# Kernel tuning notes

Measured on AMD Instinct MI355X. Metric: run time of the kernel, lower is better.

## Reference

```python
import jax, jax.numpy as jnp
import numpy as np

N = 25000      # nodes
E = 400000     # directed edges (avg degree 16)
FN = 32        # node feature dim
FE = 16        # edge feature dim
H = 16         # hidden_state_size
M = 16         # message_size
ITERS = 3      # mp_iterations


def setup_inputs() -> dict:
    key = jax.random.key(0)
    ks = jax.random.split(key, 16)
    s = 0.1
    return {
        "node_features": jax.random.normal(ks[0], (N, FN), jnp.float32),
        "edge_features": jax.random.normal(ks[1], (E, FE), jnp.float32),
        # Initial dense
        "W_init": jax.random.normal(ks[2], (FN, H), jnp.float32) * s,
        "b_init": jnp.zeros((H,), jnp.float32),
        # edge_net dense: FE -> M*H
        "W_edge": jax.random.normal(ks[3], (FE, M * H), jnp.float32) * s,
        "b_edge": jnp.zeros((M * H,), jnp.float32),
        # GRU (keras default, reset_after=True), input dim 1, units H, gate order z|r|h
        "Wi_gru": jax.random.normal(ks[4], (1, 3 * H), jnp.float32) * s,
        "Wh_gru": jax.random.normal(ks[5], (H, 3 * H), jnp.float32) * s,
        "bi_gru": jnp.zeros((3 * H,), jnp.float32),
        "bh_gru": jnp.zeros((3 * H,), jnp.float32),
        # Readout denses -> 1 output
        "W_ri": jax.random.normal(ks[6], (2 * H, 1), jnp.float32) * s,
        "b_ri": jnp.zeros((1,), jnp.float32),
        "W_rj": jax.random.normal(ks[7], (H, 1), jnp.float32) * s,
        "b_rj": jnp.zeros((1,), jnp.float32),
        # graph structure (directed edges): message to `receivers[e]` from `senders[e]`
        "receivers": jax.random.randint(ks[8], (E,), 0, N, jnp.int32),
        "senders": jax.random.randint(ks[9], (E,), 0, N, jnp.int32),
    }


def _gru_seq(seq, Wi, Wh, bi, bh):
    # seq: [N, T] sequence of scalars per node; keras GRU, reset_after=True, units=H
    n = seq.shape[0]
    xs = seq.T[:, :, None]  # [T, N, 1]
    h0 = jnp.zeros((n, H), seq.dtype)

    def step(h, x_t):
        gx = x_t @ Wi + bi            # [N, 3H]
        gh = h @ Wh + bh              # [N, 3H]
        xz, xr, xh = jnp.split(gx, 3, axis=1)
        hz, hr, hh = jnp.split(gh, 3, axis=1)
        z = jax.nn.sigmoid(xz + hz)
        r = jax.nn.sigmoid(xr + hr)
        hcand = jnp.tanh(xh + r * hh)
        h_new = z * h + (1.0 - z) * hcand
        return h_new, None

    h_final, _ = jax.lax.scan(step, h0, xs)
    return h_final


def reference(node_features, edge_features, W_init, b_init, W_edge, b_edge,
              Wi_gru, Wh_gru, bi_gru, bh_gru, W_ri, b_ri, W_rj, b_rj,
              receivers, senders):
    # Initial hidden state
    hidden0 = node_features @ W_init + b_init   # [N, H]
    hidden = hidden0

    # edge_net(edge) reshaped to per-edge matrices [E, M, H] (constant across iterations)
    edge_mats = (edge_features @ W_edge + b_edge).reshape(E, M, H)

    for _ in range(ITERS):
        h_nb = hidden[senders]                                  # [E, H]
        msg = jnp.einsum("emh,eh->em", edge_mats, h_nb)        # [E, M] matvec per edge
        messages = jax.ops.segment_sum(msg, receivers, num_segments=N)  # sum aggregation
        seq = jnp.concatenate([hidden, messages], axis=1)       # [N, H+M]
        hidden = _gru_seq(seq, Wi_gru, Wh_gru, bi_gru, bh_gru)  # [N, H]

    # Readout
    i = jnp.concatenate([hidden, hidden0], axis=1) @ W_ri + b_ri  # [N, 1]
    j = hidden @ W_rj + b_rj                                      # [N, 1]
    return jnp.sum(i * j, axis=0)                                 # [1]
```

## Files before the change

kernel.cpp:

```cpp
#include <hip/hip_runtime.h>

#define N_NODES 25000
#define N_EDGES 400000

__device__ __forceinline__ float fast_sigmoid(float x) {
    return __builtin_amdgcn_rcpf(1.0f + __expf(-x));
}
__device__ __forceinline__ float fast_tanh(float x) {
    return 1.0f - 2.0f * __builtin_amdgcn_rcpf(__expf(2.0f * x) + 1.0f);
}

#define SWZF(x, k) __int_as_float(__builtin_amdgcn_ds_swizzle(__float_as_int(x), ((k) << 10) | 0x1F))
#define BCAST16(x, t) __int_as_float(__builtin_amdgcn_ds_swizzle(__float_as_int(x), ((t) << 5) | 0x10))

#define STEPK2(k0, k1) { \
        float va = SWZF(hn, k0); float vb = SWZF(hn, k1); \
        az0 = fmaf(va, Wz[k0], az0); az1 = fmaf(vb, Wz[k1], az1); \
        ar0 = fmaf(va, Wr[k0], ar0); ar1 = fmaf(vb, Wr[k1], ar1); \
        ac0 = fmaf(va, Wc[k0], ac0); ac1 = fmaf(vb, Wc[k1], ac1); }

#define GRUSTEP(XV) { \
        float xv = (XV); \
        float v1 = SWZF(hn, 1); \
        float az0 = fmaf(xv, Wiz, cz); \
        float ar0 = fmaf(xv, Wir, cr); \
        float ac0 = bhh_; \
        az0 = fmaf(hn, Wz[0], az0); \
        ar0 = fmaf(hn, Wr[0], ar0); \
        ac0 = fmaf(hn, Wc[0], ac0); \
        float az1 = v1 * Wz[1]; \
        float ar1 = v1 * Wr[1]; \
        float ac1 = v1 * Wc[1]; \
        STEPK2(2,3)   STEPK2(4,5)   STEPK2(6,7) \
        STEPK2(8,9)   STEPK2(10,11) STEPK2(12,13) \
        STEPK2(14,15) \
        float z  = fast_sigmoid(az0 + az1); \
        float r  = fast_sigmoid(ar0 + ar1); \
        float hc = fast_tanh(fmaf(xv, Wih, bih_) + r * (ac0 + ac1)); \
        hn = fmaf(z, hn - hc, hc); }

__device__ __forceinline__ float gru32(float h_own, float msg_own, int j,
        const float* __restrict__ Wi, const float* __restrict__ Wh,
        const float* __restrict__ bi, const float* __restrict__ bh)
{
    float Wz[16], Wr[16], Wc[16];
#pragma unroll
    for (int k = 0; k < 16; ++k) {
        int l = j ^ k;
        Wz[k] = Wh[l*48 + j];
        Wr[k] = Wh[l*48 + 16 + j];
        Wc[k] = Wh[l*48 + 32 + j];
    }
    float Wiz = Wi[j], Wir = Wi[16+j], Wih = Wi[32+j];
    float cz   = bi[j] + bh[j];
    float cr   = bi[16+j] + bh[16+j];
    float bih_ = bi[32+j];
    float bhh_ = bh[32+j];

    float hn = 0.0f;
    GRUSTEP(BCAST16(h_own, 0))  GRUSTEP(BCAST16(h_own, 1))
    GRUSTEP(BCAST16(h_own, 2))  GRUSTEP(BCAST16(h_own, 3))
    GRUSTEP(BCAST16(h_own, 4))  GRUSTEP(BCAST16(h_own, 5))
    GRUSTEP(BCAST16(h_own, 6))  GRUSTEP(BCAST16(h_own, 7))
    GRUSTEP(BCAST16(h_own, 8))  GRUSTEP(BCAST16(h_own, 9))
    GRUSTEP(BCAST16(h_own, 10)) GRUSTEP(BCAST16(h_own, 11))
    GRUSTEP(BCAST16(h_own, 12)) GRUSTEP(BCAST16(h_own, 13))
    GRUSTEP(BCAST16(h_own, 14)) GRUSTEP(BCAST16(h_own, 15))
    GRUSTEP(BCAST16(msg_own, 0))  GRUSTEP(BCAST16(msg_own, 1))
    GRUSTEP(BCAST16(msg_own, 2))  GRUSTEP(BCAST16(msg_own, 3))
    GRUSTEP(BCAST16(msg_own, 4))  GRUSTEP(BCAST16(msg_own, 5))
    GRUSTEP(BCAST16(msg_own, 6))  GRUSTEP(BCAST16(msg_own, 7))
    GRUSTEP(BCAST16(msg_own, 8))  GRUSTEP(BCAST16(msg_own, 9))
    GRUSTEP(BCAST16(msg_own, 10)) GRUSTEP(BCAST16(msg_own, 11))
    GRUSTEP(BCAST16(msg_own, 12)) GRUSTEP(BCAST16(msg_own, 13))
    GRUSTEP(BCAST16(msg_own, 14)) GRUSTEP(BCAST16(msg_own, 15))
    return hn;
}

__device__ __forceinline__ float gather16(const float* __restrict__ tmp,
        int beg, int end, int j)
{
    const float* p = tmp + (size_t)beg * 16 + j;
    int d = end - beg;
    float s0 = 0.0f, s1 = 0.0f, s2 = 0.0f, s3 = 0.0f;
    int i = 0;
    for (; i + 8 <= d; i += 8) {
        float a0 = p[(i+0)*16];
        float a1 = p[(i+1)*16];
        float a2 = p[(i+2)*16];
        float a3 = p[(i+3)*16];
        float a4 = p[(i+4)*16];
        float a5 = p[(i+5)*16];
        float a6 = p[(i+6)*16];
        float a7 = p[(i+7)*16];
        s0 += a0; s1 += a1; s2 += a2; s3 += a3;
        s0 += a4; s1 += a5; s2 += a6; s3 += a7;
    }
    for (; i < d; ++i) s0 += p[i*16];
    return (s0 + s1) + (s2 + s3);
}

#define MCHUNK 256
#define MSG16(E0,E1,E2,E3) ( \
    ( fmaf((E0).w,q[3],  fmaf((E0).z,q[2],  fmaf((E0).y,q[1],  fmaf((E0).x,q[0],  qb)))) \
    + fmaf((E1).w,q[7],  fmaf((E1).z,q[6],  fmaf((E1).y,q[5],  fmaf((E1).x,q[4],  0.0f)))) ) \
  + ( fmaf((E2).w,q[11], fmaf((E2).z,q[10], fmaf((E2).y,q[9],  fmaf((E2).x,q[8],  0.0f)))) \
    + fmaf((E3).w,q[15], fmaf((E3).z,q[14], fmaf((E3).y,q[13], fmaf((E3).x,q[12], 0.0f)))) ) )

__device__ __forceinline__ void msg_phase(const float* __restrict__ h, int m,
        int tid, int blk_first, int beg, int end,
        const float* __restrict__ efp, const int* __restrict__ rp,
        const float* __restrict__ We, const float* __restrict__ be,
        const int* __restrict__ row_ptr, float* __restrict__ tmp,
        float* __restrict__ sef, int* __restrict__ srp)
{
    float q[16];
#pragma unroll
    for (int f = 0; f < 16; ++f) {
        const float4* wf = (const float4*)(We + f*256 + m*16);
        float4 a = wf[0], b = wf[1], c = wf[2], d = wf[3];
        float acc;
        acc  = a.x*h[0]  + a.y*h[1]  + a.z*h[2]  + a.w*h[3];
        acc += b.x*h[4]  + b.y*h[5]  + b.z*h[6]  + b.w*h[7];
        acc += c.x*h[8]  + c.y*h[9]  + c.z*h[10] + c.w*h[11];
        acc += d.x*h[12] + d.y*h[13] + d.z*h[14] + d.w*h[15];
        q[f] = acc;
    }
    float qb;
    {
        const float4* bf = (const float4*)(be + m*16);
        float4 a = bf[0], b = bf[1], c = bf[2], d = bf[3];
        qb  = a.x*h[0]  + a.y*h[1]  + a.z*h[2]  + a.w*h[3];
        qb += b.x*h[4]  + b.y*h[5]  + b.z*h[6]  + b.w*h[7];
        qb += c.x*h[8]  + c.y*h[9]  + c.z*h[10] + c.w*h[11];
        qb += d.x*h[12] + d.y*h[13] + d.z*h[14] + d.w*h[15];
    }

    int blk_beg = row_ptr[blk_first];
    int s1 = blk_first + 16; if (s1 > N_NODES) s1 = N_NODES;
    int blk_end = row_ptr[s1];

    for (int cbeg = blk_beg; cbeg < blk_end; cbeg += MCHUNK) {
        int cend = cbeg + MCHUNK; if (cend > blk_end) cend = blk_end;
        int nedge = cend - cbeg;
        int nfl = nedge * 4;
        __syncthreads();
        {
            const float4* gsrc = (const float4*)(efp + (size_t)cbeg * 16);
            float4* ldst = (float4*)sef;
            for (int i = tid; i < nfl; i += 256) ldst[i] = gsrc[i];
            for (int i = tid; i < nedge; i += 256) srp[i] = rp[cbeg + i];
        }
        __syncthreads();

        int lo = beg > cbeg ? beg : cbeg;
        int hi = end < cend ? end : cend;
        int i = lo;
        for (; i + 2 <= hi; i += 2) {
            const float4* l0 = (const float4*)(sef + (size_t)(i   - cbeg) * 16);
            const float4* l1 = (const float4*)(sef + (size_t)(i+1 - cbeg) * 16);
            float4 A0=l0[0], A1=l0[1], A2=l0[2], A3=l0[3];
            float4 B0=l1[0], B1=l1[1], B2=l1[2], B3=l1[3];
            int r0 = srp[i   - cbeg];
            int r1 = srp[i+1 - cbeg];
            float v0 = MSG16(A0, A1, A2, A3);
            float v1 = MSG16(B0, B1, B2, B3);
            tmp[(size_t)r0*16 + m] = v0;
            tmp[(size_t)r1*16 + m] = v1;
        }
        for (; i < hi; ++i) {
            const float4* l0 = (const float4*)(sef + (size_t)(i - cbeg) * 16);
            float4 A0=l0[0], A1=l0[1], A2=l0[2], A3=l0[3];
            int r0 = srp[i - cbeg];
            tmp[(size_t)r0*16 + m] = MSG16(A0, A1, A2, A3);
        }
    }
}

__global__ void __launch_bounds__(256) k_init(
        const float* __restrict__ nf, const float* __restrict__ Wini,
        const float* __restrict__ bini,
        float* __restrict__ hidden0, float* __restrict__ hid,
        int* __restrict__ cnt, int* __restrict__ rcnt)
{
    int gtid = blockIdx.x * 256 + threadIdx.x;
    if (gtid <= N_NODES) { cnt[gtid] = 0; rcnt[gtid] = 0; }
    int node = gtid >> 4;
    int j = gtid & 15;
    if (node >= N_NODES) return;

    const float4* nf4 = (const float4*)(nf + node * 32);
    float acc = bini[j];
#pragma unroll
    for (int g = 0; g < 8; ++g) {
        float4 v = nf4[g];
        acc = fmaf(v.x, Wini[(g*4+0)*16 + j], acc);
        acc = fmaf(v.y, Wini[(g*4+1)*16 + j], acc);
        acc = fmaf(v.z, Wini[(g*4+2)*16 + j], acc);
        acc = fmaf(v.w, Wini[(g*4+3)*16 + j], acc);
    }
    hidden0[node*16 + j] = acc;
    hid[node*16 + j] = acc;
}

__global__ void __launch_bounds__(256) k_rank(const int* __restrict__ send,
        const int* __restrict__ recv,
        int* __restrict__ cnt, int* __restrict__ rcnt,
        int* __restrict__ rank_s, int* __restrict__ rank_r)
{
    int e = blockIdx.x * 256 + threadIdx.x;
    if (e < N_EDGES) {
        rank_s[e] = atomicAdd(&cnt[send[e]], 1);
        rank_r[e] = atomicAdd(&rcnt[recv[e]], 1);
    }
}

#define SCAN_TOT 25600
__global__ void __launch_bounds__(1024) k_scan2(
        const int* __restrict__ cnt,  int* __restrict__ row_ptr,
        const int* __restrict__ rcnt, int* __restrict__ rrow_ptr,
        float* __restrict__ out)
{
    __shared__ int data[SCAN_TOT];
    __shared__ int sums[1024];
    int t = threadIdx.x;
    const int CH = 25;

    const int* SRC = blockIdx.x ? rcnt : cnt;
    int* DST = blockIdx.x ? rrow_ptr : row_ptr;

    for (int i = t; i < SCAN_TOT; i += 1024)
        data[i] = (i < N_NODES) ? SRC[i] : 0;
    __syncthreads();

    int base = t * CH;
    int s = 0;
#pragma unroll
    for (int i = 0; i < CH; ++i) s += data[base + i];
    sums[t] = s;
    __syncthreads();

    for (int off = 1; off < 1024; off <<= 1) {
        int add = (t >= off) ? sums[t - off] : 0;
        __syncthreads();
        sums[t] += add;
        __syncthreads();
    }
    int run = sums[t] - s;

#pragma unroll
    for (int i = 0; i < CH; ++i) {
        int v = data[base + i];
        data[base + i] = run;
        run += v;
    }
    __syncthreads();

    for (int i = t; i < N_NODES; i += 1024)
        DST[i] = data[i];
    if (t == 0) {
        if (blockIdx.x == 0) { row_ptr[N_NODES] = N_EDGES; out[0] = 0.0f; }
        else                 { rrow_ptr[N_NODES] = N_EDGES; }
    }
}

__global__ void __launch_bounds__(256) k_place(const int* __restrict__ send,
        const int* __restrict__ recv,
        const int* __restrict__ rank_s, const int* __restrict__ rank_r,
        const int* __restrict__ row_ptr, const int* __restrict__ rrow_ptr,
        const float* __restrict__ ef, float* __restrict__ efp,
        int* __restrict__ rp)
{
    int e = blockIdx.x * 256 + threadIdx.x;
    if (e < N_EDGES) {
        int pos = row_ptr[send[e]] + rank_s[e];
        rp[pos] = rrow_ptr[recv[e]] + rank_r[e];
        const float4* src = (const float4*)(ef + (size_t)e * 16);
        float4* dst = (float4*)(efp + (size_t)pos * 16);
        float4 a = src[0], b = src[1], c = src[2], d = src[3];
        dst[0] = a; dst[1] = b; dst[2] = c; dst[3] = d;
    }
}

__global__ void __launch_bounds__(256) k_msg(
        const float* __restrict__ hid, const float* __restrict__ efp,
        const int* __restrict__ rp,
        const float* __restrict__ We, const float* __restrict__ be,
        const int* __restrict__ row_ptr,
        float* __restrict__ tmp)
{
    __shared__ float sef[MCHUNK * 16];
    __shared__ int   srp[MCHUNK];
    int tid = threadIdx.x;
    int grp = tid >> 4;
    int m   = tid & 15;
    int s   = blockIdx.x * 16 + grp;
    bool active = (s < N_NODES);
    int sc = active ? s : 0;

    int beg = active ? row_ptr[s]     : 0;
    int end = active ? row_ptr[s + 1] : 0;

    float h[16];
    {
        const float4* h4 = (const float4*)(hid + sc*16);
        float4 a = h4[0], b = h4[1], c = h4[2], d = h4[3];
        h[0]=a.x; h[1]=a.y; h[2]=a.z;  h[3]=a.w;
        h[4]=b.x; h[5]=b.y; h[6]=b.z;  h[7]=b.w;
        h[8]=c.x; h[9]=c.y; h[10]=c.z; h[11]=c.w;
        h[12]=d.x; h[13]=d.y; h[14]=d.z; h[15]=d.w;
    }
    msg_phase(h, m, tid, blockIdx.x * 16, beg, end,
              efp, rp, We, be, row_ptr, tmp, sef, srp);
}

__global__ void __launch_bounds__(256) k_gru(
        const float* __restrict__ hid_in, const float* __restrict__ tmp,
        const int* __restrict__ rrow_ptr,
        const float* __restrict__ Wi, const float* __restrict__ Wh,
        const float* __restrict__ bi, const float* __restrict__ bh,
        float* __restrict__ hid_out)
{
    int gtid = blockIdx.x * 256 + threadIdx.x;
    int node = gtid >> 4;
    int j = gtid & 15;
    if (node >= N_NODES) return;

    float msg_own = gather16(tmp, rrow_ptr[node], rrow_ptr[node + 1], j);
    float h_own = hid_in[node*16 + j];
    float hn = gru32(h_own, msg_own, j, Wi, Wh, bi, bh);
    hid_out[node*16 + j] = hn;
}

__global__ void __launch_bounds__(256) k_fused(
        const float* __restrict__ hid_in, const float* __restrict__ tmp_in,
        const int* __restrict__ rrow_ptr,
        const float* __restrict__ Wi, const float* __restrict__ Wh,
        const float* __restrict__ bi, const float* __restrict__ bh,
        float* __restrict__ hid_out,
        const float* __restrict__ efp, const int* __restrict__ rp,
        const float* __restrict__ We, const float* __restrict__ be,
        const int* __restrict__ row_ptr, float* __restrict__ tmp_out)
{
    __shared__ float sef[MCHUNK * 16];
    __shared__ int   srp[MCHUNK];
    int tid = threadIdx.x;
    int grp = tid >> 4;
    int j   = tid & 15;
    int node = blockIdx.x * 16 + grp;
    bool active = (node < N_NODES);
    int nc = active ? node : 0;

    int gbeg = rrow_ptr[nc];
    int gend = active ? rrow_ptr[nc + 1] : gbeg;
    float msg_own = gather16(tmp_in, gbeg, gend, j);
    float h_own = hid_in[nc*16 + j];
    float hn = gru32(h_own, msg_own, j, Wi, Wh, bi, bh);
    if (active) hid_out[node*16 + j] = hn;

    float h[16];
    h[0]  = BCAST16(hn, 0);   h[1]  = BCAST16(hn, 1);
    h[2]  = BCAST16(hn, 2);   h[3]  = BCAST16(hn, 3);
    h[4]  = BCAST16(hn, 4);   h[5]  = BCAST16(hn, 5);
    h[6]  = BCAST16(hn, 6);   h[7]  = BCAST16(hn, 7);
    h[8]  = BCAST16(hn, 8);   h[9]  = BCAST16(hn, 9);
    h[10] = BCAST16(hn, 10);  h[11] = BCAST16(hn, 11);
    h[12] = BCAST16(hn, 12);  h[13] = BCAST16(hn, 13);
    h[14] = BCAST16(hn, 14);  h[15] = BCAST16(hn, 15);

    int beg = active ? row_ptr[node]     : 0;
    int end = active ? row_ptr[node + 1] : 0;
    msg_phase(h, j, tid, blockIdx.x * 16, beg, end,
              efp, rp, We, be, row_ptr, tmp_out, sef, srp);
}

__global__ void __launch_bounds__(256) k_readout(
        const float* __restrict__ hid, const float* __restrict__ hid0,
        const float* __restrict__ Wri, const float* __restrict__ bri,
        const float* __restrict__ Wrj, const float* __restrict__ brj,
        float* __restrict__ out)
{
    int n = blockIdx.x * 256 + threadIdx.x;
    float val = 0.0f;
    if (n < N_NODES) {
        const float4* h4 = (const float4*)(hid + n * 16);
        const float4* g4 = (const float4*)(hid0 + n * 16);
        float iv = bri[0];
        float jv = brj[0];
#pragma unroll
        for (int g = 0; g < 4; ++g) {
            float4 h  = h4[g];
            float4 h0 = g4[g];
            iv = fmaf(h.x,  Wri[g*4+0], iv);  iv = fmaf(h.y,  Wri[g*4+1], iv);
            iv = fmaf(h.z,  Wri[g*4+2], iv);  iv = fmaf(h.w,  Wri[g*4+3], iv);
            iv = fmaf(h0.x, Wri[16+g*4+0], iv); iv = fmaf(h0.y, Wri[16+g*4+1], iv);
            iv = fmaf(h0.z, Wri[16+g*4+2], iv); iv = fmaf(h0.w, Wri[16+g*4+3], iv);
            jv = fmaf(h.x,  Wrj[g*4+0], jv);  jv = fmaf(h.y,  Wrj[g*4+1], jv);
            jv = fmaf(h.z,  Wrj[g*4+2], jv);  jv = fmaf(h.w,  Wrj[g*4+3], jv);
        }
        val = iv * jv;
    }
#pragma unroll
    for (int off = 32; off > 0; off >>= 1)
        val += __shfl_xor(val, off, 64);
    __shared__ float wsum[4];
    int w = threadIdx.x >> 6;
    if ((threadIdx.x & 63) == 0) wsum[w] = val;
    __syncthreads();
    if (threadIdx.x == 0)
        atomicAdd(out, wsum[0] + wsum[1] + wsum[2] + wsum[3]);
}

extern "C" void kernel_launch(void* const* d_in, const int* in_sizes, int n_in,
                              void* d_out, int out_size, void* d_ws, size_t ws_size,
                              hipStream_t stream)
{
    const float* node_features = (const float*)d_in[0];
    const float* edge_features = (const float*)d_in[1];
    const float* W_init = (const float*)d_in[2];
    const float* b_init = (const float*)d_in[3];
    const float* W_edge = (const float*)d_in[4];
    const float* b_edge = (const float*)d_in[5];
    const float* Wi_gru = (const float*)d_in[6];
    const float* Wh_gru = (const float*)d_in[7];
    const float* bi_gru = (const float*)d_in[8];
    const float* bh_gru = (const float*)d_in[9];
    const float* W_ri = (const float*)d_in[10];
    const float* b_ri = (const float*)d_in[11];
    const float* W_rj = (const float*)d_in[12];
    const float* b_rj = (const float*)d_in[13];
    const int* receivers = (const int*)d_in[14];
    const int* senders   = (const int*)d_in[15];
    float* out = (float*)d_out;

    float* fb      = (float*)d_ws;
    float* hidden0 = fb;
    float* hidA    = fb + 400000;
    float* hidB    = fb + 800000;
    float* tmpA    = fb + 1200000;
    float* tmpB    = fb + 7600000;
    float* efp     = fb + 14000000;
    int* ib       = (int*)(fb + 20400000);
    int* cnt      = ib;
    int* row_ptr  = ib + 25024;
    int* rcnt     = ib + 50048;
    int* rrow_ptr = ib + 75072;
    int* rp       = ib + 100096;
    int* rank_s   = ib + 500096;
    int* rank_r   = ib + 900096;

    dim3 b256(256);
    int grid_n16 = (N_NODES * 16 + 255) / 256;
    int grid_e   = (N_EDGES + 255) / 256;
    int grid_n   = (N_NODES + 255) / 256;
    int grid_blk = (N_NODES + 15) / 16;

    k_init<<<grid_n16, b256, 0, stream>>>(node_features, W_init, b_init,
                                          hidden0, hidA, cnt, rcnt);
    k_rank<<<grid_e, b256, 0, stream>>>(senders, receivers, cnt, rcnt,
                                        rank_s, rank_r);
    k_scan2<<<2, 1024, 0, stream>>>(cnt, row_ptr, rcnt, rrow_ptr, out);
    k_place<<<grid_e, b256, 0, stream>>>(senders, receivers, rank_s, rank_r,
                                         row_ptr, rrow_ptr,
                                         edge_features, efp, rp);

    k_msg<<<grid_blk, b256, 0, stream>>>(hidA, efp, rp,
                                         W_edge, b_edge, row_ptr, tmpA);
    k_fused<<<grid_blk, b256, 0, stream>>>(hidA, tmpA, rrow_ptr,
                                           Wi_gru, Wh_gru, bi_gru, bh_gru,
                                           hidB,
                                           efp, rp, W_edge, b_edge, row_ptr,
                                           tmpB);
    k_fused<<<grid_blk, b256, 0, stream>>>(hidB, tmpB, rrow_ptr,
                                           Wi_gru, Wh_gru, bi_gru, bh_gru,
                                           hidA,
                                           efp, rp, W_edge, b_edge, row_ptr,
                                           tmpA);
    k_gru<<<grid_n16, b256, 0, stream>>>(hidA, tmpA, rrow_ptr,
                                         Wi_gru, Wh_gru, bi_gru, bh_gru, hidB);

    k_readout<<<grid_n, b256, 0, stream>>>(hidB, hidden0, W_ri, b_ri, W_rj, b_rj, out);
}
```

Measured before the change: 379.1 us.

## Fuse init dense into first message kernel and GRU into readout

The initial dense projection now runs inside the first message kernel, and its result is broadcast within each 16-lane group instead of being re-read from memory. The final GRU step and the readout reduction are merged into a single kernel, so the last hidden state is never written out. The counter zeroing moves to a memset, and the count arrays are made contiguous so one memset clears both. This cuts one or two launches and some global traffic, at the cost of more work per thread in the fused kernels.

```diff
diff --git a/kernel.cpp b/kernel.cpp
--- a/kernel.cpp
+++ b/kernel.cpp
@@ -177,32 +177,6 @@
     }
 }
 
-__global__ void __launch_bounds__(256) k_init(
-        const float* __restrict__ nf, const float* __restrict__ Wini,
-        const float* __restrict__ bini,
-        float* __restrict__ hidden0, float* __restrict__ hid,
-        int* __restrict__ cnt, int* __restrict__ rcnt)
-{
-    int gtid = blockIdx.x * 256 + threadIdx.x;
-    if (gtid <= N_NODES) { cnt[gtid] = 0; rcnt[gtid] = 0; }
-    int node = gtid >> 4;
-    int j = gtid & 15;
-    if (node >= N_NODES) return;
-
-    const float4* nf4 = (const float4*)(nf + node * 32);
-    float acc = bini[j];
-#pragma unroll
-    for (int g = 0; g < 8; ++g) {
-        float4 v = nf4[g];
-        acc = fmaf(v.x, Wini[(g*4+0)*16 + j], acc);
-        acc = fmaf(v.y, Wini[(g*4+1)*16 + j], acc);
-        acc = fmaf(v.z, Wini[(g*4+2)*16 + j], acc);
-        acc = fmaf(v.w, Wini[(g*4+3)*16 + j], acc);
-    }
-    hidden0[node*16 + j] = acc;
-    hid[node*16 + j] = acc;
-}
-
 __global__ void __launch_bounds__(256) k_rank(const int* __restrict__ send,
         const int* __restrict__ recv,
         int* __restrict__ cnt, int* __restrict__ rcnt,
@@ -282,54 +256,52 @@
     }
 }
 
-__global__ void __launch_bounds__(256) k_msg(
-        const float* __restrict__ hid, const float* __restrict__ efp,
-        const int* __restrict__ rp,
+__global__ void __launch_bounds__(256) k_init_msg(
+        const float* __restrict__ nf, const float* __restrict__ Wini,
+        const float* __restrict__ bini,
+        float* __restrict__ hidden0, float* __restrict__ hid,
+        const float* __restrict__ efp, const int* __restrict__ rp,
         const float* __restrict__ We, const float* __restrict__ be,
-        const int* __restrict__ row_ptr,
-        float* __restrict__ tmp)
+        const int* __restrict__ row_ptr, float* __restrict__ tmp)
 {
     __shared__ float sef[MCHUNK * 16];
     __shared__ int   srp[MCHUNK];
     int tid = threadIdx.x;
     int grp = tid >> 4;
-    int m   = tid & 15;
-    int s   = blockIdx.x * 16 + grp;
-    bool active = (s < N_NODES);
-    int sc = active ? s : 0;
-
-    int beg = active ? row_ptr[s]     : 0;
-    int end = active ? row_ptr[s + 1] : 0;
+    int j   = tid & 15;
+    int node = blockIdx.x * 16 + grp;
+    bool active = (node < N_NODES);
+    int nc = active ? node : 0;
+
+    const float4* nf4 = (const float4*)(nf + (size_t)nc * 32);
+    float acc = bini[j];
+#pragma unroll
+    for (int g = 0; g < 8; ++g) {
+        float4 v = nf4[g];
+        acc = fmaf(v.x, Wini[(g*4+0)*16 + j], acc);
+        acc = fmaf(v.y, Wini[(g*4+1)*16 + j], acc);
+        acc = fmaf(v.z, Wini[(g*4+2)*16 + j], acc);
+        acc = fmaf(v.w, Wini[(g*4+3)*16 + j], acc);
+    }
+    if (active) {
+        hidden0[node*16 + j] = acc;
+        hid[node*16 + j] = acc;
+    }
 
     float h[16];
-    {
-        const float4* h4 = (const float4*)(hid + sc*16);
-        float4 a = h4[0], b = h4[1], c = h4[2], d = h4[3];
-        h[0]=a.x; h[1]=a.y; h[2]=a.z;  h[3]=a.w;
-        h[4]=b.x; h[5]=b.y; h[6]=b.z;  h[7]=b.w;
-        h[8]=c.x; h[9]=c.y; h[10]=c.z; h[11]=c.w;
-        h[12]=d.x; h[13]=d.y; h[14]=d.z; h[15]=d.w;
-    }
-    msg_phase(h, m, tid, blockIdx.x * 16, beg, end,
+    h[0]  = BCAST16(acc, 0);   h[1]  = BCAST16(acc, 1);
+    h[2]  = BCAST16(acc, 2);   h[3]  = BCAST16(acc, 3);
+    h[4]  = BCAST16(acc, 4);   h[5]  = BCAST16(acc, 5);
+    h[6]  = BCAST16(acc, 6);   h[7]  = BCAST16(acc, 7);
+    h[8]  = BCAST16(acc, 8);   h[9]  = BCAST16(acc, 9);
+    h[10] = BCAST16(acc, 10);  h[11] = BCAST16(acc, 11);
+    h[12] = BCAST16(acc, 12);  h[13] = BCAST16(acc, 13);
+    h[14] = BCAST16(acc, 14);  h[15] = BCAST16(acc, 15);
+
+    int beg = active ? row_ptr[node]     : 0;
+    int end = active ? row_ptr[node + 1] : 0;
+    msg_phase(h, j, tid, blockIdx.x * 16, beg, end,
               efp, rp, We, be, row_ptr, tmp, sef, srp);
-}
-
-__global__ void __launch_bounds__(256) k_gru(
-        const float* __restrict__ hid_in, const float* __restrict__ tmp,
-        const int* __restrict__ rrow_ptr,
-        const float* __restrict__ Wi, const float* __restrict__ Wh,
-        const float* __restrict__ bi, const float* __restrict__ bh,
-        float* __restrict__ hid_out)
-{
-    int gtid = blockIdx.x * 256 + threadIdx.x;
-    int node = gtid >> 4;
-    int j = gtid & 15;
-    if (node >= N_NODES) return;
-
-    float msg_own = gather16(tmp, rrow_ptr[node], rrow_ptr[node + 1], j);
-    float h_own = hid_in[node*16 + j];
-    float hn = gru32(h_own, msg_own, j, Wi, Wh, bi, bh);
-    hid_out[node*16 + j] = hn;
 }
 
 __global__ void __launch_bounds__(256) k_fused(
@@ -374,32 +346,38 @@
               efp, rp, We, be, row_ptr, tmp_out, sef, srp);
 }
 
-__global__ void __launch_bounds__(256) k_readout(
-        const float* __restrict__ hid, const float* __restrict__ hid0,
+__global__ void __launch_bounds__(256) k_gru_red(
+        const float* __restrict__ hid_in, const float* __restrict__ tmp,
+        const int* __restrict__ rrow_ptr,
+        const float* __restrict__ Wi, const float* __restrict__ Wh,
+        const float* __restrict__ bi, const float* __restrict__ bh,
+        const float* __restrict__ hid0,
         const float* __restrict__ Wri, const float* __restrict__ bri,
         const float* __restrict__ Wrj, const float* __restrict__ brj,
         float* __restrict__ out)
 {
-    int n = blockIdx.x * 256 + threadIdx.x;
-    float val = 0.0f;
-    if (n < N_NODES) {
-        const float4* h4 = (const float4*)(hid + n * 16);
-        const float4* g4 = (const float4*)(hid0 + n * 16);
-        float iv = bri[0];
-        float jv = brj[0];
-#pragma unroll
-        for (int g = 0; g < 4; ++g) {
-            float4 h  = h4[g];
-            float4 h0 = g4[g];
-            iv = fmaf(h.x,  Wri[g*4+0], iv);  iv = fmaf(h.y,  Wri[g*4+1], iv);
-            iv = fmaf(h.z,  Wri[g*4+2], iv);  iv = fmaf(h.w,  Wri[g*4+3], iv);
-            iv = fmaf(h0.x, Wri[16+g*4+0], iv); iv = fmaf(h0.y, Wri[16+g*4+1], iv);
-            iv = fmaf(h0.z, Wri[16+g*4+2], iv); iv = fmaf(h0.w, Wri[16+g*4+3], iv);
-            jv = fmaf(h.x,  Wrj[g*4+0], jv);  jv = fmaf(h.y,  Wrj[g*4+1], jv);
-            jv = fmaf(h.z,  Wrj[g*4+2], jv);  jv = fmaf(h.w,  Wrj[g*4+3], jv);
-        }
-        val = iv * jv;
-    }
+    int gtid = blockIdx.x * 256 + threadIdx.x;
+    int node = gtid >> 4;
+    int j = gtid & 15;
+    bool active = (node < N_NODES);
+    int nc = active ? node : 0;
+
+    int gbeg = rrow_ptr[nc];
+    int gend = active ? rrow_ptr[nc + 1] : gbeg;
+    float msg_own = gather16(tmp, gbeg, gend, j);
+    float h_own = hid_in[nc*16 + j];
+    float hn = gru32(h_own, msg_own, j, Wi, Wh, bi, bh);
+
+    float h0 = hid0[nc*16 + j];
+    float pi = fmaf(hn, Wri[j], h0 * Wri[16 + j]);
+    float pj = hn * Wrj[j];
+    if (j == 0) { pi += bri[0]; pj += brj[0]; }
+    pi += SWZF(pi, 1);  pj += SWZF(pj, 1);
+    pi += SWZF(pi, 2);  pj += SWZF(pj, 2);
+    pi += SWZF(pi, 4);  pj += SWZF(pj, 4);
+    pi += SWZF(pi, 8);  pj += SWZF(pj, 8);
+
+    float val = (active && j == 0) ? pi * pj : 0.0f;
 #pragma unroll
     for (int off = 32; off > 0; off >>= 1)
         val += __shfl_xor(val, off, 64);
@@ -442,21 +420,19 @@
     float* efp     = fb + 14000000;
     int* ib       = (int*)(fb + 20400000);
     int* cnt      = ib;
-    int* row_ptr  = ib + 25024;
-    int* rcnt     = ib + 50048;
+    int* rcnt     = ib + 25024;
+    int* row_ptr  = ib + 50048;
     int* rrow_ptr = ib + 75072;
     int* rp       = ib + 100096;
     int* rank_s   = ib + 500096;
     int* rank_r   = ib + 900096;
 
     dim3 b256(256);
+    int grid_e   = (N_EDGES + 255) / 256;
     int grid_n16 = (N_NODES * 16 + 255) / 256;
-    int grid_e   = (N_EDGES + 255) / 256;
-    int grid_n   = (N_NODES + 255) / 256;
     int grid_blk = (N_NODES + 15) / 16;
 
-    k_init<<<grid_n16, b256, 0, stream>>>(node_features, W_init, b_init,
-                                          hidden0, hidA, cnt, rcnt);
+    hipMemsetAsync(cnt, 0, 2 * 25024 * sizeof(int), stream);
     k_rank<<<grid_e, b256, 0, stream>>>(senders, receivers, cnt, rcnt,
                                         rank_s, rank_r);
     k_scan2<<<2, 1024, 0, stream>>>(cnt, row_ptr, rcnt, rrow_ptr, out);
@@ -464,8 +440,10 @@
                                          row_ptr, rrow_ptr,
                                          edge_features, efp, rp);
 
-    k_msg<<<grid_blk, b256, 0, stream>>>(hidA, efp, rp,
-                                         W_edge, b_edge, row_ptr, tmpA);
+    k_init_msg<<<grid_blk, b256, 0, stream>>>(node_features, W_init, b_init,
+                                              hidden0, hidA,
+                                              efp, rp, W_edge, b_edge, row_ptr,
+                                              tmpA);
     k_fused<<<grid_blk, b256, 0, stream>>>(hidA, tmpA, rrow_ptr,
                                            Wi_gru, Wh_gru, bi_gru, bh_gru,
                                            hidB,
@@ -476,8 +454,8 @@
                                            hidA,
                                            efp, rp, W_edge, b_edge, row_ptr,
                                            tmpA);
-    k_gru<<<grid_n16, b256, 0, stream>>>(hidA, tmpA, rrow_ptr,
-                                         Wi_gru, Wh_gru, bi_gru, bh_gru, hidB);
-
-    k_readout<<<grid_n, b256, 0, stream>>>(hidB, hidden0, W_ri, b_ri, W_rj, b_rj, out);
-}
+    k_gru_red<<<grid_n16, b256, 0, stream>>>(hidA, tmpA, rrow_ptr,
+                                             Wi_gru, Wh_gru, bi_gru, bh_gru,
+                                             hidden0,
+                                             W_ri, b_ri, W_rj, b_rj, out);
+}
```

Result: no change. 375.4 us (-1.0%).
